# Kernel tuning notes

Hardware: AMD Instinct MI355X
Metric: run time of the kernel (lower is better)

The kernel has to match this reference:

```python
import jax, jax.numpy as jnp
import numpy as np

C_IN, LAT, OUT, EMB = 3, 64, 512, 5
B, H = 128, 128
KS = [4, 4, 3, 4, 2]                       # per-layer dynamic kernel sizes
CHANS = [C_IN, LAT, LAT * 2, LAT * 4, LAT * 8]  # in-channels of each dyn conv
MIX = [(C_IN, LAT), (LAT, LAT * 2), (LAT * 2, LAT * 4), (LAT * 4, LAT * 8), (LAT * 8, OUT)]


def setup_inputs() -> dict:
    key = jax.random.key(0)
    ks = jax.random.split(key, 40)
    nrm = lambda k, shape, s=0.02: jax.random.normal(k, shape, jnp.float32) * s
    inp = {}
    inp["input"] = jax.random.normal(ks[0], (B, C_IN, H, H), jnp.float32)
    inp["label"] = jax.random.randint(ks[1], (B,), 0, 10)
    inp["emb"] = nrm(ks[2], (10, EMB), 1.0)  # label embedding table
    i = 3
    for j, (c, k) in enumerate(zip(CHANS, KS), 1):  # label -> dyn kernel linears
        inp[f"l{j}_w"] = nrm(ks[i], (EMB, c * k * k), 0.1)
        inp[f"l{j}_b"] = jnp.zeros((c * k * k,), jnp.float32)
        i += 1
    for j, (ci, co) in enumerate(MIX, 1):  # channel-mixer linears
        inp[f"cm{j}_w"] = nrm(ks[i], (ci, co))
        inp[f"cm{j}_b"] = jnp.zeros((co,), jnp.float32)
        i += 1
    for j, c in enumerate([LAT, LAT * 2, LAT * 4, LAT * 8], 1):  # BN affine params
        inp[f"bn{j}_g"] = jnp.ones((c,), jnp.float32)
        inp[f"bn{j}_b"] = jnp.zeros((c,), jnp.float32)
    return inp


def dw_conv(x, k, stride, pad):
    """Per-sample, per-channel (depthwise) 2d cross-correlation.
    x: (B,C,H,W), k: (B,C,h,w) -> (B,C,H',W')."""
    def one(xi, ki):
        return jax.lax.conv_general_dilated(
            xi[None], ki[:, None], (stride, stride),
            [(pad, pad), (pad, pad)],
            dimension_numbers=("NCHW", "OIHW", "NCHW"),
            feature_group_count=xi.shape[0])[0]
    return jax.vmap(one)(x, k)


def reference(input, label, emb,
              l1_w, l1_b, l2_w, l2_b, l3_w, l3_b, l4_w, l4_b, l5_w, l5_b,
              cm1_w, cm1_b, cm2_w, cm2_b, cm3_w, cm3_b, cm4_w, cm4_b, cm5_w, cm5_b,
              bn1_g, bn1_b, bn2_g, bn2_b, bn3_g, bn3_b, bn4_g, bn4_b):
    e = emb[label]  # (B, EMB)
    dk = lambda w, b, c, k: jnp.tanh(e @ w + b).reshape(-1, c, k, k)
    k1 = dk(l1_w, l1_b, C_IN, 4)
    k2 = dk(l2_w, l2_b, LAT, 4)
    k3 = dk(l3_w, l3_b, LAT * 2, 3)
    k4 = dk(l4_w, l4_b, LAT * 4, 4)
    k5 = dk(l5_w, l5_b, LAT * 8, 2)

    mix = lambda z, w, b: jnp.einsum("bchw,cd->bdhw", z, w) + b[None, :, None, None]
    lrelu = lambda z: jax.nn.leaky_relu(z, 0.2)

    def bn(z, g, b):  # training-mode BN (batch statistics, biased var, eps=1e-5)
        m = z.mean((0, 2, 3), keepdims=True)
        v = z.var((0, 2, 3), keepdims=True)
        return (z - m) * jax.lax.rsqrt(v + 1e-5) * g[None, :, None, None] + b[None, :, None, None]

    z = bn(lrelu(mix(dw_conv(input, k1, 2, 1), cm1_w, cm1_b)), bn1_g, bn1_b)
    z = bn(lrelu(mix(dw_conv(z, k2, 2, 1), cm2_w, cm2_b)), bn2_g, bn2_b)
    z = bn(lrelu(mix(dw_conv(z, k3, 2, 1), cm3_w, cm3_b)), bn3_g, bn3_b)
    z = bn(lrelu(mix(dw_conv(z, k4, 2, 1), cm4_w, cm4_b)), bn4_g, bn4_b)
    z = jax.nn.sigmoid(mix(dw_conv(z, k5, 1, 0), cm5_w, cm5_b))  # (B, OUT, 7, 7)
    return (z, label)
```

## Files before the change

### kernel.cpp

```cpp
#include <hip/hip_runtime.h>
#include <hip/hip_bf16.h>

typedef __hip_bfloat16 bf16;
using short8  = __attribute__((ext_vector_type(8))) short;
using floatx4 = __attribute__((ext_vector_type(4))) float;

__device__ __forceinline__ float b2f(unsigned short u) {
    union { unsigned int i; float f; } v; v.i = ((unsigned int)u) << 16; return v.f;
}
__device__ __forceinline__ unsigned short f2b(float f) {
    bf16 h = __float2bfloat16(f);
    return *(unsigned short*)&h;
}

#define NREP 16

__global__ __launch_bounds__(256) void prep_kernel(
    const int* __restrict__ label, const float* __restrict__ emb,
    const float* __restrict__ l1w, const float* __restrict__ l1b,
    const float* __restrict__ l2w, const float* __restrict__ l2b,
    const float* __restrict__ l3w, const float* __restrict__ l3b,
    const float* __restrict__ l4w, const float* __restrict__ l4b,
    const float* __restrict__ l5w, const float* __restrict__ l5b,
    float* __restrict__ dynk, float* __restrict__ stats,
    float* __restrict__ labelOut)
{
    const int tid = threadIdx.x;
    if (blockIdx.x == gridDim.x - 1) {
        for (int i = tid; i < 30720; i += 256) stats[i] = 0.0f;
        if (tid < 128) labelOut[tid] = (float)label[tid];
        return;
    }
    int idx = blockIdx.x * 256 + tid;
    if (idx >= 1071104) return;
    const float* w; const float* bb; int loc, ckk;
    if (idx < 6144)        { w = l1w; bb = l1b; loc = idx;          ckk = 48;   }
    else if (idx < 137216) { w = l2w; bb = l2b; loc = idx - 6144;   ckk = 1024; }
    else if (idx < 284672) { w = l3w; bb = l3b; loc = idx - 137216; ckk = 1152; }
    else if (idx < 808960) { w = l4w; bb = l4b; loc = idx - 284672; ckk = 4096; }
    else                   { w = l5w; bb = l5b; loc = idx - 808960; ckk = 2048; }
    int b   = loc / ckk;
    int col = loc - b * ckk;
    int lab = label[b];
    float acc = bb[col];
    #pragma unroll
    for (int m = 0; m < 5; ++m)
        acc = fmaf(emb[lab * 5 + m], w[m * ckk + col], acc);
    dynk[idx] = tanhf(acc);
}

__global__ __launch_bounds__(256) void wt_kernel(
    const float* __restrict__ w2, const float* __restrict__ w3,
    const float* __restrict__ w4, const float* __restrict__ w5,
    bf16* __restrict__ wt2, bf16* __restrict__ wt3,
    bf16* __restrict__ wt4, bf16* __restrict__ wt5)
{
    __shared__ float T[32][33];
    const int tid = threadIdx.x;
    int t = blockIdx.x;
    const float* W; bf16* WT; int K, N, tl;
    if (t < 8)        { W = w2; WT = wt2; K = 64;  N = 128; tl = t; }
    else if (t < 40)  { W = w3; WT = wt3; K = 128; N = 256; tl = t - 8; }
    else if (t < 168) { W = w4; WT = wt4; K = 256; N = 512; tl = t - 40; }
    else              { W = w5; WT = wt5; K = 512; N = 512; tl = t - 168; }
    const int NT = N >> 5;
    const int kt = tl / NT, nt = tl - kt * NT;
    const int k0 = kt * 32, n0 = nt * 32;
    const int cc = tid & 31, rr = tid >> 5;
    #pragma unroll
    for (int it = 0; it < 4; ++it) {
        int k = rr + it * 8;
        T[k][cc] = W[(long)(k0 + k) * N + n0 + cc];
    }
    __syncthreads();
    #pragma unroll
    for (int it = 0; it < 4; ++it) {
        int n = rr + it * 8;
        WT[(long)(n0 + n) * K + k0 + cc] = __float2bfloat16(T[cc][n]);
    }
}

__global__ __launch_bounds__(128) void fused_l1_v3(
    const float* __restrict__ xf, const float* __restrict__ dynk,
    const float* __restrict__ W, const float* __restrict__ bias,
    bf16* __restrict__ y, float* __restrict__ statsOut)
{
    constexpr int HIN = 128, HOUT = 64;
    constexpr int TW = 16, TH = 8;
    constexpr int PS  = 36;
    constexpr int PCH = 18 * PS;

    __shared__ float patch[3 * PCH];
    __shared__ __align__(16) float dwT[16 * 28];
    __shared__ float Wlds[192];
    __shared__ float klds[48];
    __shared__ float biasL[64];
    __shared__ float sums[64], sqs[64];

    const int tid = threadIdx.x;
    const int b   = blockIdx.x >> 5;
    const int tl  = blockIdx.x & 31;
    const int ty0 = (tl >> 2) * TH;
    const int tx0 = (tl & 3) * TW;

    if (tid < 48) klds[tid] = dynk[b * 48 + tid];
    for (int i = tid; i < 192; i += 128) Wlds[i] = W[i];
    if (tid < 64) { biasL[tid] = bias[tid]; sums[tid] = 0.f; sqs[tid] = 0.f; }

    {
        const int iy0 = ty0 * 2 - 1, ix0 = tx0 * 2 - 1;
        for (int i = tid; i < 3 * 18 * 34; i += 128) {
            int c  = i / 612;
            int r  = i - c * 612;
            int py = r / 34, px = r - py * 34;
            int gy = iy0 + py, gx = ix0 + px;
            float v = 0.f;
            if ((unsigned)gy < (unsigned)HIN && (unsigned)gx < (unsigned)HIN)
                v = xf[((long)b * 3 + c) * (HIN * HIN) + gy * HIN + gx];
            patch[c * PCH + py * PS + px] = v;
        }
    }
    __syncthreads();

    {
        const int py = tid >> 4, px = tid & 15;
        const int pixg = tid >> 3, j = tid & 7;
        #pragma unroll
        for (int c = 0; c < 3; ++c) {
            const float* pb = &patch[c * PCH + (py * 2) * PS + px * 2];
            float a = 0.f;
            #pragma unroll
            for (int kh = 0; kh < 4; ++kh)
                #pragma unroll
                for (int kw = 0; kw < 4; ++kw)
                    a = fmaf(pb[kh * PS + kw], klds[c * 16 + kh * 4 + kw], a);
            dwT[pixg * 28 + j * 3 + c] = a;
        }
    }
    __syncthreads();

    {
        const int cq = tid & 7, pixg = tid >> 3;
        const int d0 = cq * 8;
        float Wr[3][8], bi[8];
        #pragma unroll
        for (int c = 0; c < 3; ++c)
            #pragma unroll
            for (int t = 0; t < 8; ++t) Wr[c][t] = Wlds[c * 64 + d0 + t];
        #pragma unroll
        for (int t = 0; t < 8; ++t) bi[t] = biasL[d0 + t];

        float dv[24];
        #pragma unroll
        for (int q4 = 0; q4 < 6; ++q4)
            *(float4*)&dv[q4 * 4] = *(const float4*)&dwT[pixg * 28 + q4 * 4];

        float sreg[8] = {}, qreg[8] = {};
        #pragma unroll
        for (int j = 0; j < 8; ++j) {
            const int pos = pixg * 8 + j;
            const float dv0 = dv[j * 3 + 0];
            const float dv1 = dv[j * 3 + 1];
            const float dv2 = dv[j * 3 + 2];
            const int py = pos >> 4, px = pos & 15;
            const long row = ((long)(b * HOUT + ty0 + py)) * HOUT + tx0 + px;
            union { uint4 v; unsigned short us[8]; } pk;
            #pragma unroll
            for (int t = 0; t < 8; ++t) {
                float v = fmaf(dv0, Wr[0][t], fmaf(dv1, Wr[1][t], fmaf(dv2, Wr[2][t], bi[t])));
                v = v > 0.f ? v : 0.2f * v;
                sreg[t] += v;
                qreg[t] = fmaf(v, v, qreg[t]);
                pk.us[t] = f2b(v);
            }
            *(uint4*)&y[row * 64 + d0] = pk.v;
        }
        #pragma unroll
        for (int m = 8; m < 64; m <<= 1)
            #pragma unroll
            for (int t = 0; t < 8; ++t) {
                sreg[t] += __shfl_xor(sreg[t], m);
                qreg[t] += __shfl_xor(qreg[t], m);
            }
        if ((tid & 63) < 8) {
            #pragma unroll
            for (int t = 0; t < 8; ++t) {
                atomicAdd(&sums[d0 + t], sreg[t]);
                atomicAdd(&sqs [d0 + t], qreg[t]);
            }
        }
    }
    __syncthreads();
    {
        const int rep = blockIdx.x & (NREP - 1);
        if (tid < 64) {
            atomicAdd(&statsOut[rep * 128 + tid],      sums[tid]);
            atomicAdd(&statsOut[rep * 128 + 64 + tid], sqs[tid]);
        }
    }
}

template<int C, int KS, int HIN, int HOUT, int STRIDE, int PAD, int OXPT, int OYPB, int NTHR>
__global__ __launch_bounds__(NTHR) void dw_tiled(
    const bf16* __restrict__ x, const float* __restrict__ st,
    const float* __restrict__ gam, const float* __restrict__ bet,
    const float* __restrict__ dynk, bf16* __restrict__ outA, float NINV)
{
    constexpr int G    = C / 8;
    constexpr int OXG  = HOUT / OXPT;
    constexpr int NIX  = (OXPT - 1) * STRIDE + KS;
    constexpr int KSK  = KS * KS;
    static_assert(NTHR == OYPB * OXG * G, "thread count mismatch");

    __shared__ float wlds[KSK * C];
    __shared__ float scaleL[C], shiftL[C];

    const int tid = threadIdx.x;
    const int bpb = HOUT / OYPB;
    const int b   = blockIdx.x / bpb;
    const int oy0 = (blockIdx.x % bpb) * OYPB;

    for (int i = tid; i < KSK * C; i += NTHR) {
        int c = i / KSK, t = i - c * KSK;
        wlds[t * C + c] = dynk[((long)b * C + c) * KSK + t];
    }
    for (int c = tid; c < C; c += NTHR) {
        float s = 0.f, q = 0.f;
        #pragma unroll
        for (int r = 0; r < NREP; ++r) {
            s += st[r * 2 * C + c];
            q += st[r * 2 * C + C + c];
        }
        float m   = s * NINV;
        float var = fmaf(q, NINV, -m * m);
        float scv = gam[c] * rsqrtf(var + 1e-5f);
        scaleL[c] = scv;
        shiftL[c] = fmaf(-m, scv, bet[c]);
    }
    __syncthreads();

    const int g   = tid % G;
    const int rs  = tid / G;
    const int oxg = rs % OXG;
    const int oy  = oy0 + rs / OXG;
    const int c0  = g * 8;

    float sc[8], sh[8];
    #pragma unroll
    for (int j = 0; j < 8; ++j) { sc[j] = scaleL[c0 + j]; sh[j] = shiftL[c0 + j]; }

    float acc[OXPT][8];
    #pragma unroll
    for (int p = 0; p < OXPT; ++p)
        #pragma unroll
        for (int ch = 0; ch < 8; ++ch) acc[p][ch] = 0.f;

    const int ix0 = oxg * OXPT * STRIDE - PAD;

    #pragma unroll
    for (int kh = 0; kh < KS; ++kh) {
        const int iy = oy * STRIDE - PAD + kh;
        const bool rowOK = ((unsigned)iy < (unsigned)HIN);
        uint4 xr[NIX];
        #pragma unroll
        for (int i = 0; i < NIX; ++i) {
            int ix = ix0 + i;
            uint4 v; v.x = 0u; v.y = 0u; v.z = 0u; v.w = 0u;
            if (rowOK && (unsigned)ix < (unsigned)HIN)
                v = *(const uint4*)&x[((long)(b * HIN + iy) * HIN + ix) * C + c0];
            xr[i] = v;
        }
        #pragma unroll
        for (int kw = 0; kw < KS; ++kw) {
            float4 wa = *(const float4*)&wlds[(kh * KS + kw) * C + c0];
            float4 wb = *(const float4*)&wlds[(kh * KS + kw) * C + c0 + 4];
            const float wt[8] = {wa.x, wa.y, wa.z, wa.w, wb.x, wb.y, wb.z, wb.w};
            #pragma unroll
            for (int pos = 0; pos < OXPT; ++pos) {
                const int i  = pos * STRIDE + kw;
                const int ix = ix0 + i;
                const bool ok = rowOK && ((unsigned)ix < (unsigned)HIN);
                const uint4& xv = xr[i];
                #pragma unroll
                for (int ch = 0; ch < 8; ++ch) {
                    unsigned u = ((const unsigned*)&xv)[ch >> 1];
                    unsigned bits = (ch & 1) ? (u & 0xffff0000u) : (u << 16);
                    float xb = ok ? fmaf(__uint_as_float(bits), sc[ch], sh[ch]) : 0.f;
                    acc[pos][ch] = fmaf(xb, wt[ch], acc[pos][ch]);
                }
            }
        }
    }

    #pragma unroll
    for (int pos = 0; pos < OXPT; ++pos) {
        const int ox = oxg * OXPT + pos;
        union { uint4 v; unsigned short us[8]; } pk;
        #pragma unroll
        for (int ch = 0; ch < 8; ++ch)
            pk.us[ch] = f2b(acc[pos][ch]);
        *(uint4*)&outA[((long)(b * HOUT + oy) * HOUT + ox) * C + c0] = pk.v;
    }
}

template<int K, int COUT, bool LAST>
__global__ __launch_bounds__(256) void gemm_layer(
    const bf16* __restrict__ A, const bf16* __restrict__ WT,
    const float* __restrict__ bias, bf16* __restrict__ y,
    float* __restrict__ statsOut, float* __restrict__ outF, int Mtiles)
{
    constexpr int SK = 72;
    constexpr int CS = 136;
    __shared__ __align__(16) unsigned short smem[18432];
    unsigned short* As  = smem;
    unsigned short* Bs  = smem + 9216;
    unsigned short* Csh = smem;
    __shared__ float sums[128], sqs[128];

    const int tid  = threadIdx.x;
    const int lane = tid & 63;
    const int w    = tid >> 6;
    const int wm   = (w >> 1) * 64, wn = (w & 1) * 64;
    const int lm   = lane & 15, lq = lane >> 4;
    const int mt   = blockIdx.x % Mtiles;
    const int nt   = blockIdx.x / Mtiles;
    const long m0  = (long)mt * 128;
    const int  n0  = nt * 128;

    floatx4 acc[4][4];
    #pragma unroll
    for (int i = 0; i < 4; ++i)
        #pragma unroll
        for (int j = 0; j < 4; ++j) acc[i][j] = (floatx4)0.0f;

    for (int kb = 0; kb < K; kb += 64) {
        __syncthreads();
        #pragma unroll
        for (int s = 0; s < 4; ++s) {
            int i = tid + s * 256;
            int m = i >> 3, q = i & 7;
            uint4 va = *(const uint4*)(A  + ((m0 + m) * K + kb + q * 8));
            uint4 vb = *(const uint4*)(WT + ((long)(n0 + m) * K + kb + q * 8));
            *(uint4*)&As[m * SK + q * 8] = va;
            *(uint4*)&Bs[m * SK + q * 8] = vb;
        }
        __syncthreads();
        #pragma unroll
        for (int h = 0; h < 2; ++h) {
            short8 af[4], bfr[4];
            #pragma unroll
            for (int i = 0; i < 4; ++i) {
                af[i]  = *(const short8*)&As[(wm + i * 16 + lm) * SK + h * 32 + lq * 8];
                bfr[i] = *(const short8*)&Bs[(wn + i * 16 + lm) * SK + h * 32 + lq * 8];
            }
            #pragma unroll
            for (int i = 0; i < 4; ++i)
                #pragma unroll
                for (int j = 0; j < 4; ++j)
                    acc[i][j] = __builtin_amdgcn_mfma_f32_16x16x32_bf16(af[i], bfr[j], acc[i][j], 0, 0, 0);
        }
    }
    __syncthreads();

    float bj[4];
    #pragma unroll
    for (int j = 0; j < 4; ++j) bj[j] = bias[n0 + wn + j * 16 + lm];

    if constexpr (!LAST) {
        if (tid < 128) { sums[tid] = 0.f; sqs[tid] = 0.f; }
        #pragma unroll
        for (int i = 0; i < 4; ++i)
            #pragma unroll
            for (int j = 0; j < 4; ++j) {
                int c = wn + j * 16 + lm;
                #pragma unroll
                for (int rg = 0; rg < 4; ++rg) {
                    int r = wm + i * 16 + lq * 4 + rg;
                    float v = acc[i][j][rg] + bj[j];
                    v = v > 0.f ? v : 0.2f * v;
                    Csh[r * CS + c] = f2b(v);
                }
            }
        __syncthreads();
        const int cg = tid & 15, mr = tid >> 4;
        float sacc[8], qacc[8];
        #pragma unroll
        for (int t = 0; t < 8; ++t) { sacc[t] = 0.f; qacc[t] = 0.f; }
        #pragma unroll
        for (int it = 0; it < 8; ++it) {
            int m = mr + it * 16;
            uint4 pk = *(const uint4*)&Csh[m * CS + cg * 8];
            *(uint4*)&y[(m0 + m) * COUT + n0 + cg * 8] = pk;
            const unsigned short* pu = (const unsigned short*)&pk;
            #pragma unroll
            for (int t = 0; t < 8; ++t) {
                float f = b2f(pu[t]);
                sacc[t] += f;
                qacc[t] = fmaf(f, f, qacc[t]);
            }
        }
        #pragma unroll
        for (int t = 0; t < 8; ++t) {
            atomicAdd(&sums[cg * 8 + t], sacc[t]);
            atomicAdd(&sqs [cg * 8 + t], qacc[t]);
        }
        __syncthreads();
        {
            const int rep = blockIdx.x & (NREP - 1);
            if (tid < 128) {
                atomicAdd(&statsOut[rep * 2 * COUT + n0 + tid],        sums[tid]);
                atomicAdd(&statsOut[rep * 2 * COUT + COUT + n0 + tid], sqs[tid]);
            }
        }
    } else {
        #pragma unroll
        for (int i = 0; i < 4; ++i)
            #pragma unroll
            for (int j = 0; j < 4; ++j) {
                int c  = wn + j * 16 + lm;
                int rb = wm + i * 16 + lq * 4;
                ushort4 pk;
                unsigned short* pp = (unsigned short*)&pk;
                #pragma unroll
                for (int rg = 0; rg < 4; ++rg)
                    pp[rg] = f2b(acc[i][j][rg] + bj[j]);
                *(ushort4*)&Csh[c * CS + rb] = pk;
            }
        __syncthreads();
        const int mg = tid & 15, nr = tid >> 4;
        #pragma unroll
        for (int it = 0; it < 8; ++it) {
            int n = nr + it * 16;
            uint4 pk = *(const uint4*)&Csh[n * CS + mg * 8];
            const unsigned short* pu = (const unsigned short*)&pk;
            #pragma unroll
            for (int t = 0; t < 8; ++t) {
                int m = (int)m0 + mg * 8 + t;
                int b = m / 49, pos = m - b * 49;
                float v = b2f(pu[t]);
                outF[((long)(b * 512 + n0 + n)) * 49 + pos] = 1.f / (1.f + __expf(-v));
            }
        }
    }
}


extern "C" void kernel_launch(void* const* d_in, const int* in_sizes, int n_in,
                              void* d_out, int out_size, void* d_ws, size_t ws_size,
                              hipStream_t stream)
{
    const float* input = (const float*)d_in[0];
    const int*   label = (const int*)d_in[1];
    const float* emb   = (const float*)d_in[2];
    const float* lw[5] = {(const float*)d_in[3], (const float*)d_in[5], (const float*)d_in[7],
                          (const float*)d_in[9], (const float*)d_in[11]};
    const float* lb[5] = {(const float*)d_in[4], (const float*)d_in[6], (const float*)d_in[8],
                          (const float*)d_in[10], (const float*)d_in[12]};
    const float* cmw[5] = {(const float*)d_in[13], (const float*)d_in[15], (const float*)d_in[17],
                           (const float*)d_in[19], (const float*)d_in[21]};
    const float* cmb[5] = {(const float*)d_in[14], (const float*)d_in[16], (const float*)d_in[18],
                           (const float*)d_in[20], (const float*)d_in[22]};
    const float* bng[4] = {(const float*)d_in[23], (const float*)d_in[25],
                           (const float*)d_in[27], (const float*)d_in[29]};
    const float* bnb[4] = {(const float*)d_in[24], (const float*)d_in[26],
                           (const float*)d_in[28], (const float*)d_in[30]};
    float* out = (float*)d_out;

    float* wsf   = (float*)d_ws;
    float* dynk  = wsf;
    float* stats = wsf + 1071104;
    const float* k1 = dynk;
    const float* k2 = dynk + 6144;
    const float* k3 = dynk + 137216;
    const float* k4 = dynk + 284672;
    const float* k5 = dynk + 808960;
    float* st1 = stats;
    float* st2 = stats + 2048;
    float* st3 = stats + 6144;
    float* st4 = stats + 14336;

    bf16* wt  = (bf16*)((char*)d_ws + 4407296);
    bf16* wt2 = wt;
    bf16* wt3 = wt + 8192;
    bf16* wt4 = wt + 40960;
    bf16* wt5 = wt + 172032;
    bf16* S1  = (bf16*)((char*)d_ws + 5308416);
    bf16* S2  = (bf16*)((char*)d_ws + 72417280);

    prep_kernel<<<4186, 256, 0, stream>>>(label, emb,
        lw[0], lb[0], lw[1], lb[1], lw[2], lb[2], lw[3], lb[3], lw[4], lb[4],
        dynk, stats, out + 3211264);
    wt_kernel<<<424, 256, 0, stream>>>(cmw[1], cmw[2], cmw[3], cmw[4],
                                       wt2, wt3, wt4, wt5);

    fused_l1_v3<<<4096, 128, 0, stream>>>(input, k1, cmw[0], cmb[0], S1, st1);

    dw_tiled<64, 4, 64, 32, 2, 1, 4, 4, 256><<<1024, 256, 0, stream>>>(
        S1, st1, bng[0], bnb[0], k2, S2, 1.f / 524288.f);
    gemm_layer<64, 128, false><<<1024, 256, 0, stream>>>(
        S2, wt2, cmb[1], S1, st2, nullptr, 1024);

    dw_tiled<128, 3, 32, 16, 2, 1, 4, 4, 256><<<512, 256, 0, stream>>>(
        S1, st2, bng[1], bnb[1], k3, S2, 1.f / 131072.f);
    gemm_layer<128, 256, false><<<512, 256, 0, stream>>>(
        S2, wt3, cmb[2], S1, st3, nullptr, 256);

    dw_tiled<256, 4, 16, 8, 2, 1, 4, 4, 256><<<256, 256, 0, stream>>>(
        S1, st3, bng[2], bnb[2], k4, S2, 1.f / 32768.f);
    gemm_layer<256, 512, false><<<256, 256, 0, stream>>>(
        S2, wt4, cmb[3], S1, st4, nullptr, 64);

    dw_tiled<512, 2, 8, 7, 1, 0, 7, 7, 448><<<128, 448, 0, stream>>>(
        S1, st4, bng[3], bnb[3], k5, S2, 1.f / 8192.f);
    gemm_layer<512, 512, true><<<196, 256, 0, stream>>>(
        S2, wt5, cmb[4], nullptr, nullptr, out, 49);
}
```

Measured before the change: 358.5 us.

## Replace tiled depthwise conv with one-row-per-block direct conv and folded BN

Each depthwise-conv block now computes a single output row, with one output pixel per thread across 8 channels, and launches 4-7x more blocks. Interior pixels skip the per-tap BN affine: the raw sum is scaled once and shift times the kernel-weight sum is added, using a new precomputed per-channel weight sum. Border pixels keep the per-tap normalize path with skipped out-of-range taps. The cost is losing input reuse across horizontal output positions, since each thread loads its own window, and every block now reloads the dynamic weights and BN statistics.

Result: faster. 342.4 us (-4.5%).

```diff
diff --git a/kernel.cpp b/kernel.cpp
--- a/kernel.cpp
+++ b/kernel.cpp
@@ -200,25 +200,23 @@
     }
 }
 
-template<int C, int KS, int HIN, int HOUT, int STRIDE, int PAD, int OXPT, int OYPB, int NTHR>
-__global__ __launch_bounds__(NTHR) void dw_tiled(
+template<int C, int KS, int HIN, int HOUT, int STRIDE, int PAD, int NTHR>
+__global__ __launch_bounds__(NTHR) void dw_direct(
     const bf16* __restrict__ x, const float* __restrict__ st,
     const float* __restrict__ gam, const float* __restrict__ bet,
     const float* __restrict__ dynk, bf16* __restrict__ outA, float NINV)
 {
-    constexpr int G    = C / 8;
-    constexpr int OXG  = HOUT / OXPT;
-    constexpr int NIX  = (OXPT - 1) * STRIDE + KS;
-    constexpr int KSK  = KS * KS;
-    static_assert(NTHR == OYPB * OXG * G, "thread count mismatch");
+    constexpr int G   = C / 8;
+    constexpr int KSK = KS * KS;
+    static_assert(NTHR == HOUT * G, "one output row per block");
 
     __shared__ float wlds[KSK * C];
+    __shared__ float ksumL[C];
     __shared__ float scaleL[C], shiftL[C];
 
     const int tid = threadIdx.x;
-    const int bpb = HOUT / OYPB;
-    const int b   = blockIdx.x / bpb;
-    const int oy0 = (blockIdx.x % bpb) * OYPB;
+    const int b   = blockIdx.x / HOUT;
+    const int oy  = blockIdx.x % HOUT;
 
     for (int i = tid; i < KSK * C; i += NTHR) {
         int c = i / KSK, t = i - c * KSK;
@@ -238,69 +236,85 @@
         shiftL[c] = fmaf(-m, scv, bet[c]);
     }
     __syncthreads();
-
-    const int g   = tid % G;
-    const int rs  = tid / G;
-    const int oxg = rs % OXG;
-    const int oy  = oy0 + rs / OXG;
-    const int c0  = g * 8;
-
-    float sc[8], sh[8];
-    #pragma unroll
-    for (int j = 0; j < 8; ++j) { sc[j] = scaleL[c0 + j]; sh[j] = shiftL[c0 + j]; }
-
-    float acc[OXPT][8];
-    #pragma unroll
-    for (int p = 0; p < OXPT; ++p)
-        #pragma unroll
-        for (int ch = 0; ch < 8; ++ch) acc[p][ch] = 0.f;
-
-    const int ix0 = oxg * OXPT * STRIDE - PAD;
-
-    #pragma unroll
-    for (int kh = 0; kh < KS; ++kh) {
-        const int iy = oy * STRIDE - PAD + kh;
-        const bool rowOK = ((unsigned)iy < (unsigned)HIN);
-        uint4 xr[NIX];
-        #pragma unroll
-        for (int i = 0; i < NIX; ++i) {
-            int ix = ix0 + i;
-            uint4 v; v.x = 0u; v.y = 0u; v.z = 0u; v.w = 0u;
-            if (rowOK && (unsigned)ix < (unsigned)HIN)
-                v = *(const uint4*)&x[((long)(b * HIN + iy) * HIN + ix) * C + c0];
-            xr[i] = v;
-        }
-        #pragma unroll
-        for (int kw = 0; kw < KS; ++kw) {
-            float4 wa = *(const float4*)&wlds[(kh * KS + kw) * C + c0];
-            float4 wb = *(const float4*)&wlds[(kh * KS + kw) * C + c0 + 4];
-            const float wt[8] = {wa.x, wa.y, wa.z, wa.w, wb.x, wb.y, wb.z, wb.w};
-            #pragma unroll
-            for (int pos = 0; pos < OXPT; ++pos) {
-                const int i  = pos * STRIDE + kw;
-                const int ix = ix0 + i;
-                const bool ok = rowOK && ((unsigned)ix < (unsigned)HIN);
-                const uint4& xv = xr[i];
+    for (int c = tid; c < C; c += NTHR) {
+        float s = 0.f;
+        #pragma unroll
+        for (int t = 0; t < KSK; ++t) s += wlds[t * C + c];
+        ksumL[c] = s;
+    }
+    __syncthreads();
+
+    const int g  = tid % G;
+    const int ox = tid / G;
+    const int c0 = g * 8;
+    const int iy0 = oy * STRIDE - PAD;
+    const int ix0 = ox * STRIDE - PAD;
+
+    float acc[8];
+    #pragma unroll
+    for (int ch = 0; ch < 8; ++ch) acc[ch] = 0.f;
+
+    const bool interior = (iy0 >= 0) && (iy0 + KS <= HIN) &&
+                          (ix0 >= 0) && (ix0 + KS <= HIN);
+    float r[8];
+
+    if (interior) {
+        const bf16* bp = x + ((long)(b * HIN + iy0) * HIN + ix0) * C + c0;
+        #pragma unroll
+        for (int kh = 0; kh < KS; ++kh)
+            #pragma unroll
+            for (int kw = 0; kw < KS; ++kw) {
+                uint4 v = *(const uint4*)(bp + (kh * HIN + kw) * C);
+                const float* wp = &wlds[(kh * KS + kw) * C + c0];
+                float4 wa = *(const float4*)wp;
+                float4 wb = *(const float4*)(wp + 4);
+                const float wt[8] = {wa.x, wa.y, wa.z, wa.w, wb.x, wb.y, wb.z, wb.w};
                 #pragma unroll
                 for (int ch = 0; ch < 8; ++ch) {
-                    unsigned u = ((const unsigned*)&xv)[ch >> 1];
+                    unsigned u = ((const unsigned*)&v)[ch >> 1];
                     unsigned bits = (ch & 1) ? (u & 0xffff0000u) : (u << 16);
-                    float xb = ok ? fmaf(__uint_as_float(bits), sc[ch], sh[ch]) : 0.f;
-                    acc[pos][ch] = fmaf(xb, wt[ch], acc[pos][ch]);
+                    acc[ch] = fmaf(__uint_as_float(bits), wt[ch], acc[ch]);
                 }
             }
-        }
-    }
-
-    #pragma unroll
-    for (int pos = 0; pos < OXPT; ++pos) {
-        const int ox = oxg * OXPT + pos;
-        union { uint4 v; unsigned short us[8]; } pk;
-        #pragma unroll
-        for (int ch = 0; ch < 8; ++ch)
-            pk.us[ch] = f2b(acc[pos][ch]);
-        *(uint4*)&outA[((long)(b * HOUT + oy) * HOUT + ox) * C + c0] = pk.v;
-    }
+        #pragma unroll
+        for (int ch = 0; ch < 8; ++ch) {
+            float sc = scaleL[c0 + ch], sh = shiftL[c0 + ch], ks = ksumL[c0 + ch];
+            r[ch] = fmaf(sc, acc[ch], sh * ks);
+        }
+    } else {
+        float sc[8], sh[8];
+        #pragma unroll
+        for (int ch = 0; ch < 8; ++ch) { sc[ch] = scaleL[c0 + ch]; sh[ch] = shiftL[c0 + ch]; }
+        #pragma unroll
+        for (int kh = 0; kh < KS; ++kh) {
+            const int iy = iy0 + kh;
+            if ((unsigned)iy >= (unsigned)HIN) continue;
+            #pragma unroll
+            for (int kw = 0; kw < KS; ++kw) {
+                const int ix = ix0 + kw;
+                if ((unsigned)ix >= (unsigned)HIN) continue;
+                uint4 v = *(const uint4*)&x[((long)(b * HIN + iy) * HIN + ix) * C + c0];
+                const float* wp = &wlds[(kh * KS + kw) * C + c0];
+                float4 wa = *(const float4*)wp;
+                float4 wb = *(const float4*)(wp + 4);
+                const float wt[8] = {wa.x, wa.y, wa.z, wa.w, wb.x, wb.y, wb.z, wb.w};
+                #pragma unroll
+                for (int ch = 0; ch < 8; ++ch) {
+                    unsigned u = ((const unsigned*)&v)[ch >> 1];
+                    unsigned bits = (ch & 1) ? (u & 0xffff0000u) : (u << 16);
+                    float xb = fmaf(__uint_as_float(bits), sc[ch], sh[ch]);
+                    acc[ch] = fmaf(xb, wt[ch], acc[ch]);
+                }
+            }
+        }
+        #pragma unroll
+        for (int ch = 0; ch < 8; ++ch) r[ch] = acc[ch];
+    }
+
+    union { uint4 v; unsigned short us[8]; } pk;
+    #pragma unroll
+    for (int ch = 0; ch < 8; ++ch) pk.us[ch] = f2b(r[ch]);
+    *(uint4*)&outA[((long)(b * HOUT + oy) * HOUT + ox) * C + c0] = pk.v;
 }
 
 template<int K, int COUT, bool LAST>
@@ -495,22 +509,22 @@
 
     fused_l1_v3<<<4096, 128, 0, stream>>>(input, k1, cmw[0], cmb[0], S1, st1);
 
-    dw_tiled<64, 4, 64, 32, 2, 1, 4, 4, 256><<<1024, 256, 0, stream>>>(
+    dw_direct<64, 4, 64, 32, 2, 1, 256><<<4096, 256, 0, stream>>>(
         S1, st1, bng[0], bnb[0], k2, S2, 1.f / 524288.f);
     gemm_layer<64, 128, false><<<1024, 256, 0, stream>>>(
         S2, wt2, cmb[1], S1, st2, nullptr, 1024);
 
-    dw_tiled<128, 3, 32, 16, 2, 1, 4, 4, 256><<<512, 256, 0, stream>>>(
+    dw_direct<128, 3, 32, 16, 2, 1, 256><<<2048, 256, 0, stream>>>(
         S1, st2, bng[1], bnb[1], k3, S2, 1.f / 131072.f);
     gemm_layer<128, 256, false><<<512, 256, 0, stream>>>(
         S2, wt3, cmb[2], S1, st3, nullptr, 256);
 
-    dw_tiled<256, 4, 16, 8, 2, 1, 4, 4, 256><<<256, 256, 0, stream>>>(
+    dw_direct<256, 4, 16, 8, 2, 1, 256><<<1024, 256, 0, stream>>>(
         S1, st3, bng[2], bnb[2], k4, S2, 1.f / 32768.f);
     gemm_layer<256, 512, false><<<256, 256, 0, stream>>>(
         S2, wt4, cmb[3], S1, st4, nullptr, 64);
 
-    dw_tiled<512, 2, 8, 7, 1, 0, 7, 7, 448><<<128, 448, 0, stream>>>(
+    dw_direct<512, 2, 8, 7, 1, 0, 448><<<896, 448, 0, stream>>>(
         S1, st4, bng[3], bnb[3], k5, S2, 1.f / 8192.f);
     gemm_layer<512, 512, true><<<196, 256, 0, stream>>>(
         S2, wt5, cmb[4], nullptr, nullptr, out, 49);
```
